# Kernel optimization log

Hardware: AMD Instinct MI355X
Metric: run time of the kernel (lower is better)

## Reference

```python
import jax, jax.numpy as jnp
import numpy as np

B, N, DS, DP, H, DH = 2, 512, 384, 128, 16, 64
MAX_SEQ = 2048
DI = H * DH  # inner attention dim = 1024
LN_EPS = 1e-5


def setup_inputs() -> dict:
    key = jax.random.key(0)
    ks = jax.random.split(key, 10)
    s = 0.02  # param init scale
    return {
        "single_repr": jax.random.normal(ks[0], (B, N, DS), jnp.float32),
        "pairwise_repr": jax.random.normal(ks[1], (B, N, N, DP), jnp.float32),
        "ln_gamma": jnp.ones((DP,), jnp.float32),
        "ln_beta": jnp.zeros((DP,), jnp.float32),
        "w_bias": jax.random.normal(ks[2], (DP, H), jnp.float32) * s,
        "attn_bias_bias": jax.random.normal(ks[3], (MAX_SEQ, MAX_SEQ), jnp.float32) * s,
        "w_q": jax.random.normal(ks[4], (DS, DI), jnp.float32) * s,
        "w_k": jax.random.normal(ks[5], (DS, DI), jnp.float32) * s,
        "w_v": jax.random.normal(ks[6], (DS, DI), jnp.float32) * s,
        "w_g": jax.random.normal(ks[7], (DS, DI), jnp.float32) * s,
        "w_o": jax.random.normal(ks[8], (DI, DS), jnp.float32) * s,
    }


def reference(single_repr, pairwise_repr, ln_gamma, ln_beta, w_bias,
              attn_bias_bias, w_q, w_k, w_v, w_g, w_o):
    b, n, _ = single_repr.shape
    # LayerNorm over pairwise feature dim, then project to per-head bias
    mu = pairwise_repr.mean(-1, keepdims=True)
    var = pairwise_repr.var(-1, keepdims=True)
    pr = (pairwise_repr - mu) * jax.lax.rsqrt(var + LN_EPS) * ln_gamma + ln_beta
    # ... i j h -> ... h i j, plus learned positional bias slice
    attn_bias = jnp.einsum('bijd,dh->bhij', pr, w_bias) + attn_bias_bias[:n, :n]

    # multi-head attention with additive per-head bias and sigmoid gating
    q = (single_repr @ w_q).reshape(b, n, H, DH).transpose(0, 2, 1, 3)  # bhnd
    k = (single_repr @ w_k).reshape(b, n, H, DH).transpose(0, 2, 1, 3)
    v = (single_repr @ w_v).reshape(b, n, H, DH).transpose(0, 2, 1, 3)
    scale = DH ** -0.5
    scores = jnp.einsum('bhid,bhjd->bhij', q, k) * scale + attn_bias
    attn = jax.nn.softmax(scores, axis=-1)
    o = jnp.einsum('bhij,bhjd->bhid', attn, v)
    o = o.transpose(0, 2, 1, 3).reshape(b, n, DI)
    gates = jax.nn.sigmoid(single_repr @ w_g)
    return (o * gates) @ w_o
```

## Files before the change

### kernel.cpp

```cpp
#include <hip/hip_runtime.h>
#include <hip/hip_bf16.h>

#define B_ 2
#define N_ 512
#define DS_ 384
#define DP_ 128
#define H_ 16
#define DH_ 64
#define DI_ 1024
#define MAXSEQ 2048
#define PAD 8

typedef float f32x4 __attribute__((ext_vector_type(4)));
typedef short bf16x8 __attribute__((ext_vector_type(8)));

__device__ __forceinline__ unsigned short f2b(float f) {
    unsigned int u = __builtin_bit_cast(unsigned int, f);
    u += 0x7FFFu + ((u >> 16) & 1u);
    return (unsigned short)(u >> 16);
}
__device__ __forceinline__ float b2f(unsigned short s) {
    unsigned int u = ((unsigned int)s) << 16;
    return __builtin_bit_cast(float, u);
}

__global__ __launch_bounds__(256) void k_transpose_all(const float* __restrict__ wq,
                                                       const float* __restrict__ wk,
                                                       const float* __restrict__ wv,
                                                       const float* __restrict__ wg,
                                                       const float* __restrict__ wo,
                                                       const float* __restrict__ gamma,
                                                       const float* __restrict__ beta,
                                                       const float* __restrict__ wb,
                                                       unsigned short* __restrict__ Wt,
                                                       unsigned short* __restrict__ Wot,
                                                       unsigned short* __restrict__ GhG,
                                                       float* __restrict__ SsG,
                                                       float* __restrict__ TsG) {
    int z = blockIdx.z;
    if (z == 5) {
        if (blockIdx.x || blockIdx.y) return;
        int t = threadIdx.x;
        for (int idx = t; idx < DP_ * H_; idx += 256) {
            int d = idx >> 4, h = idx & 15;
            GhG[h * DP_ + d] = f2b(gamma[d] * wb[idx]);
        }
        if (t < 32) {
            int h = t & 15;
            const float* src = (t >= 16) ? beta : gamma;
            float s = 0.f;
            for (int d = 0; d < DP_; ++d) s = fmaf(src[d], wb[d * H_ + h], s);
            if (t >= 16) TsG[h] = s; else SsG[h] = s;
        }
        return;
    }
    __shared__ float tile[32][33];
    const float* in;
    unsigned short* out;
    int R, C;
    if (z < 4) {
        in = (z == 0) ? wq : (z == 1) ? wk : (z == 2) ? wv : wg;
        out = Wt + (long)z * 1024 * 384;
        R = 384; C = 1024;
    } else {
        in = wo; out = Wot; R = 1024; C = 384;
    }
    int c0 = blockIdx.x * 32, r0 = blockIdx.y * 32;
    if (c0 >= C || r0 >= R) return;
    int tx = threadIdx.x & 31, ty = threadIdx.x >> 5;
    #pragma unroll
    for (int i = ty; i < 32; i += 8)
        tile[i][tx] = in[(long)(r0 + i) * C + (c0 + tx)];
    __syncthreads();
    #pragma unroll
    for (int i = ty; i < 32; i += 8)
        out[(long)(c0 + i) * R + (r0 + tx)] = f2b(tile[tx][i]);
}

__global__ __launch_bounds__(256) void k_bias(const float* __restrict__ pw,
                                              const float* __restrict__ abb,
                                              const unsigned short* __restrict__ GhG,
                                              const float* __restrict__ SsG,
                                              const float* __restrict__ TsG,
                                              unsigned short* __restrict__ biasP) {
    __shared__ float Xs[64 * 128];
    __shared__ float rsum[4][16] __attribute__((aligned(16)));
    __shared__ float rsq[4][16] __attribute__((aligned(16)));
    int t = threadIdx.x;
    int w = t >> 6, lane = t & 63;
    int lane15 = lane & 15, kg = lane >> 4;
    long p0 = (long)blockIdx.x * 64;
    int i_blk = (int)((p0 >> 9) & (N_ - 1));
    int j0 = (int)(p0 & (N_ - 1));
    long bb = p0 >> 18;

    const char* src = (const char*)(pw + (p0 << 7));
    char* lds = (char*)Xs;
    #pragma unroll
    for (int c = 0; c < 8; ++c) {
        int L = c * 4096 + t * 16;
        int row = L >> 9, b = L & 511;
        uint4 v = *(const uint4*)(src + L);
        *(uint4*)(lds + (row << 9) + (b ^ ((row & 7) << 4))) = v;
    }

    bf16x8 gb[4];
    #pragma unroll
    for (int kk = 0; kk < 4; ++kk)
        gb[kk] = *(const bf16x8*)&GhG[lane15 * DP_ + kk * 32 + kg * 8];
    float sh = SsG[lane15], th = TsG[lane15];
    __syncthreads();

    int row = w * 16 + lane15;
    const char* rbase = lds + (row << 9);
    int sw = (lane15 & 7) << 4;
    f32x4 xa[4], xb4[4];
    #pragma unroll
    for (int kk = 0; kk < 4; ++kk) {
        int b0 = kk * 128 + kg * 32;
        xa[kk]  = *(const f32x4*)(rbase + ((b0) ^ sw));
        xb4[kk] = *(const f32x4*)(rbase + ((b0 + 16) ^ sw));
    }
    float s = 0.f, q = 0.f;
    #pragma unroll
    for (int kk = 0; kk < 4; ++kk) {
        s += xa[kk][0] + xa[kk][1] + xa[kk][2] + xa[kk][3];
        s += xb4[kk][0] + xb4[kk][1] + xb4[kk][2] + xb4[kk][3];
        #pragma unroll
        for (int e = 0; e < 4; ++e) {
            q = fmaf(xa[kk][e], xa[kk][e], q);
            q = fmaf(xb4[kk][e], xb4[kk][e], q);
        }
    }
    s += __shfl_xor(s, 16); s += __shfl_xor(s, 32);
    q += __shfl_xor(q, 16); q += __shfl_xor(q, 32);
    if (lane < 16) { rsum[w][lane15] = s; rsq[w][lane15] = q; }

    f32x4 acc = {};
    #pragma unroll
    for (int kk = 0; kk < 4; ++kk) {
        bf16x8 a;
        unsigned short* ap = (unsigned short*)&a;
        ap[0] = f2b(xa[kk][0]);  ap[1] = f2b(xa[kk][1]);
        ap[2] = f2b(xa[kk][2]);  ap[3] = f2b(xa[kk][3]);
        ap[4] = f2b(xb4[kk][0]); ap[5] = f2b(xb4[kk][1]);
        ap[6] = f2b(xb4[kk][2]); ap[7] = f2b(xb4[kk][3]);
        acc = __builtin_amdgcn_mfma_f32_16x16x32_bf16(a, gb[kk], acc, 0, 0, 0);
    }
    int jr = w * 16 + kg * 4;
    float4 rs = *(const float4*)&rsum[w][kg * 4];
    float4 rq = *(const float4*)&rsq[w][kg * 4];
    float4 av = *(const float4*)(abb + (long)i_blk * MAXSEQ + j0 + jr);
    unsigned short* planeBase = biasP + ((bb * H_ + lane15) * N_ + i_blk) * N_ + j0;
    ushort4 res;
    float mu, var;
    mu = rs.x * (1.f / DP_); var = fmaf(rq.x, 1.f / DP_, -mu * mu);
    res.x = f2b(fmaf(rsqrtf(var + 1e-5f), acc[0] - mu * sh, th + av.x));
    mu = rs.y * (1.f / DP_); var = fmaf(rq.y, 1.f / DP_, -mu * mu);
    res.y = f2b(fmaf(rsqrtf(var + 1e-5f), acc[1] - mu * sh, th + av.y));
    mu = rs.z * (1.f / DP_); var = fmaf(rq.z, 1.f / DP_, -mu * mu);
    res.z = f2b(fmaf(rsqrtf(var + 1e-5f), acc[2] - mu * sh, th + av.z));
    mu = rs.w * (1.f / DP_); var = fmaf(rq.w, 1.f / DP_, -mu * mu);
    res.w = f2b(fmaf(rsqrtf(var + 1e-5f), acc[3] - mu * sh, th + av.w));
    *(ushort4*)(planeBase + jr) = res;
}

__global__ __launch_bounds__(256) void k_proj(const float* __restrict__ X,
                                              const unsigned short* __restrict__ Wt,
                                              unsigned short* __restrict__ Qb,
                                              unsigned short* __restrict__ Kb,
                                              unsigned short* __restrict__ Vt,
                                              unsigned short* __restrict__ Xg) {
    __shared__ unsigned short As[128][64 + PAD];
    __shared__ unsigned short Bs[128][64 + PAD];
    int m0 = blockIdx.x * 128;
    int n0 = blockIdx.y * 128;
    int t = threadIdx.x;
    int wave = t >> 6, lane = t & 63;
    int wr = wave >> 1, wc = wave & 1;
    int lane15 = lane & 15, kg = lane >> 4;
    f32x4 acc[4][4] = {};
    for (int k0 = 0; k0 < DS_; k0 += 64) {
        __syncthreads();
        {
            int r = t >> 1, half = t & 1;
            const float4* src = (const float4*)(X + (long)(m0 + r) * DS_ + k0 + half * 32);
            unsigned short* dst = &As[r][half * 32];
            #pragma unroll
            for (int ii = 0; ii < 8; ++ii) {
                float4 v = src[ii];
                dst[ii * 4 + 0] = f2b(v.x); dst[ii * 4 + 1] = f2b(v.y);
                dst[ii * 4 + 2] = f2b(v.z); dst[ii * 4 + 3] = f2b(v.w);
            }
            const uint4* wsrc = (const uint4*)(Wt + (long)(n0 + r) * DS_ + k0 + half * 32);
            uint4* wdst = (uint4*)&Bs[r][half * 32];
            wdst[0] = wsrc[0]; wdst[1] = wsrc[1]; wdst[2] = wsrc[2]; wdst[3] = wsrc[3];
        }
        __syncthreads();
        #pragma unroll
        for (int ks = 0; ks < 2; ++ks) {
            bf16x8 a[4], bb[4];
            #pragma unroll
            for (int mf = 0; mf < 4; ++mf)
                a[mf] = *(const bf16x8*)&As[wr * 64 + mf * 16 + lane15][ks * 32 + kg * 8];
            #pragma unroll
            for (int nf = 0; nf < 4; ++nf)
                bb[nf] = *(const bf16x8*)&Bs[wc * 64 + nf * 16 + lane15][ks * 32 + kg * 8];
            #pragma unroll
            for (int mf = 0; mf < 4; ++mf)
                #pragma unroll
                for (int nf = 0; nf < 4; ++nf)
                    acc[mf][nf] = __builtin_amdgcn_mfma_f32_16x16x32_bf16(a[mf], bb[nf], acc[mf][nf], 0, 0, 0);
        }
    }
    int p = n0 >> 10;
    int lgrp = lane >> 4;
    #pragma unroll
    for (int mf = 0; mf < 4; ++mf) {
        #pragma unroll
        for (int nf = 0; nf < 4; ++nf) {
            int col = n0 + wc * 64 + nf * 16 + lane15;
            int ch = col & 1023;
            int h = ch >> 6, dh = ch & 63;
            int row0 = m0 + wr * 64 + mf * 16 + lgrp * 4;
            if (p == 0 || p == 1) {
                unsigned short* base = (p == 0) ? Qb : Kb;
                float scl = (p == 0) ? 0.125f : 1.0f;
                #pragma unroll
                for (int r = 0; r < 4; ++r) {
                    int row = row0 + r;
                    int b = row >> 9, n = row & 511;
                    base[(((long)(b * 16 + h)) * 512 + n) * 64 + dh] = f2b(acc[mf][nf][r] * scl);
                }
            } else if (p == 2) {
                int b = row0 >> 9, n = row0 & 511;
                ushort4 v;
                v.x = f2b(acc[mf][nf][0]); v.y = f2b(acc[mf][nf][1]);
                v.z = f2b(acc[mf][nf][2]); v.w = f2b(acc[mf][nf][3]);
                *(ushort4*)&Vt[(((long)(b * 16 + h)) * 64 + dh) * 512 + n] = v;
            } else {
                #pragma unroll
                for (int r = 0; r < 4; ++r) {
                    int row = row0 + r;
                    Xg[(long)row * 1024 + ch] = f2b(acc[mf][nf][r]);
                }
            }
        }
    }
}

__global__ __launch_bounds__(256) void k_flash(const unsigned short* __restrict__ Qb,
                                               const unsigned short* __restrict__ Kb,
                                               const unsigned short* __restrict__ Vt,
                                               const unsigned short* __restrict__ biasP,
                                               const unsigned short* __restrict__ Xg,
                                               unsigned short* __restrict__ Og) {
    __shared__ unsigned short Kt[64][72];
    __shared__ unsigned short Vs[64][72];
    __shared__ unsigned short Bt[64][72];
    __shared__ unsigned short Ps[4][16][72];
    int bh = blockIdx.y;
    int b = bh >> 4, h = bh & 15;
    int i0 = blockIdx.x * 64;
    int t = threadIdx.x, w = t >> 6, lane = t & 63;
    int lane15 = lane & 15, lgrp = lane >> 4;

    bf16x8 qf[2];
    #pragma unroll
    for (int kk = 0; kk < 2; ++kk)
        qf[kk] = *(const bf16x8*)&Qb[((long)bh * 512 + i0 + w * 16 + lane15) * 64 + kk * 32 + lgrp * 8];

    float m_run = -1e30f, l_run = 0.f;
    f32x4 o[4] = {};

    for (int jt = 0; jt < 8; ++jt) {
        int j0 = jt * 64;
        __syncthreads();
        #pragma unroll
        for (int i = 0; i < 2; ++i) {
            int f = i * 256 + t;
            int r = f >> 3, c = f & 7;
            *(uint4*)&Kt[r][c * 8] = *(const uint4*)&Kb[((long)bh * 512 + j0 + r) * 64 + c * 8];
            *(uint4*)&Vs[r][c * 8] = *(const uint4*)&Vt[((long)bh * 64 + r) * 512 + j0 + c * 8];
            *(uint4*)&Bt[r][c * 8] = *(const uint4*)&biasP[(((long)bh * 512) + i0 + r) * 512 + j0 + c * 8];
        }
        __syncthreads();

        f32x4 s[4];
        #pragma unroll
        for (int nf = 0; nf < 4; ++nf) {
            f32x4 z = {};
            #pragma unroll
            for (int kk = 0; kk < 2; ++kk) {
                bf16x8 af = *(const bf16x8*)&Kt[nf * 16 + lane15][kk * 32 + lgrp * 8];
                z = __builtin_amdgcn_mfma_f32_16x16x32_bf16(af, qf[kk], z, 0, 0, 0);
            }
            s[nf] = z;
        }
        #pragma unroll
        for (int nf = 0; nf < 4; ++nf)
            #pragma unroll
            for (int r = 0; r < 4; ++r)
                s[nf][r] += b2f(Bt[w * 16 + lane15][nf * 16 + lgrp * 4 + r]);

        float pmax = s[0][0];
        #pragma unroll
        for (int nf = 0; nf < 4; ++nf)
            #pragma unroll
            for (int r = 0; r < 4; ++r) pmax = fmaxf(pmax, s[nf][r]);
        pmax = fmaxf(pmax, __shfl_xor(pmax, 16));
        pmax = fmaxf(pmax, __shfl_xor(pmax, 32));
        float m_new = fmaxf(m_run, pmax);
        float scale = __expf(m_run - m_new);
        float psum = 0.f;
        #pragma unroll
        for (int nf = 0; nf < 4; ++nf)
            #pragma unroll
            for (int r = 0; r < 4; ++r) {
                s[nf][r] = __expf(s[nf][r] - m_new);
                psum += s[nf][r];
            }
        psum += __shfl_xor(psum, 16);
        psum += __shfl_xor(psum, 32);
        l_run = l_run * scale + psum;
        m_run = m_new;
        #pragma unroll
        for (int r = 0; r < 4; ++r) {
            float sc = __shfl(scale, lgrp * 4 + r);
            #pragma unroll
            for (int nf = 0; nf < 4; ++nf) o[nf][r] *= sc;
        }
        #pragma unroll
        for (int nf = 0; nf < 4; ++nf)
            #pragma unroll
            for (int r = 0; r < 4; ++r)
                Ps[w][lane15][nf * 16 + lgrp * 4 + r] = f2b(s[nf][r]);
        #pragma unroll
        for (int kk = 0; kk < 2; ++kk) {
            bf16x8 pa = *(const bf16x8*)&Ps[w][lane15][kk * 32 + lgrp * 8];
            #pragma unroll
            for (int nf = 0; nf < 4; ++nf) {
                bf16x8 vb = *(const bf16x8*)&Vs[nf * 16 + lane15][kk * 32 + lgrp * 8];
                o[nf] = __builtin_amdgcn_mfma_f32_16x16x32_bf16(pa, vb, o[nf], 0, 0, 0);
            }
        }
    }
    #pragma unroll
    for (int r = 0; r < 4; ++r) {
        float l_r = __shfl(l_run, lgrp * 4 + r);
        float inv = 1.f / l_r;
        long grow = (long)b * 512 + i0 + w * 16 + lgrp * 4 + r;
        #pragma unroll
        for (int nf = 0; nf < 4; ++nf) {
            int dh = nf * 16 + lane15;
            float xgv = b2f(Xg[grow * 1024 + h * 64 + dh]);
            float gate = 1.f / (1.f + __expf(-xgv));
            Og[grow * 1024 + h * 64 + dh] = f2b(o[nf][r] * inv * gate);
        }
    }
}

__global__ __launch_bounds__(256) void k_out(const unsigned short* __restrict__ Og,
                                             const unsigned short* __restrict__ Wot,
                                             float* __restrict__ out) {
    __shared__ unsigned short As[128][64 + PAD];
    __shared__ unsigned short Bs[128][64 + PAD];
    int m0 = blockIdx.x * 128, n0 = blockIdx.y * 128;
    int t = threadIdx.x, wave = t >> 6, lane = t & 63;
    int wr = wave >> 1, wc = wave & 1;
    int lane15 = lane & 15, kg = lane >> 4;
    f32x4 acc[4][4] = {};
    for (int k0 = 0; k0 < 1024; k0 += 64) {
        __syncthreads();
        {
            int r = t >> 1, half = t & 1;
            const uint4* src = (const uint4*)(Og + (long)(m0 + r) * 1024 + k0 + half * 32);
            uint4* dst = (uint4*)&As[r][half * 32];
            dst[0] = src[0]; dst[1] = src[1]; dst[2] = src[2]; dst[3] = src[3];
            const uint4* wsrc = (const uint4*)(Wot + (long)(n0 + r) * 1024 + k0 + half * 32);
            uint4* wdst = (uint4*)&Bs[r][half * 32];
            wdst[0] = wsrc[0]; wdst[1] = wsrc[1]; wdst[2] = wsrc[2]; wdst[3] = wsrc[3];
        }
        __syncthreads();
        #pragma unroll
        for (int ks = 0; ks < 2; ++ks) {
            bf16x8 a[4], bb[4];
            #pragma unroll
            for (int mf = 0; mf < 4; ++mf)
                a[mf] = *(const bf16x8*)&As[wr * 64 + mf * 16 + lane15][ks * 32 + kg * 8];
            #pragma unroll
            for (int nf = 0; nf < 4; ++nf)
                bb[nf] = *(const bf16x8*)&Bs[wc * 64 + nf * 16 + lane15][ks * 32 + kg * 8];
            #pragma unroll
            for (int mf = 0; mf < 4; ++mf)
                #pragma unroll
                for (int nf = 0; nf < 4; ++nf)
                    acc[mf][nf] = __builtin_amdgcn_mfma_f32_16x16x32_bf16(a[mf], bb[nf], acc[mf][nf], 0, 0, 0);
        }
    }
    int lgrp = lane >> 4;
    #pragma unroll
    for (int mf = 0; mf < 4; ++mf) {
        #pragma unroll
        for (int nf = 0; nf < 4; ++nf) {
            int col = n0 + wc * 64 + nf * 16 + lane15;
            int row0 = m0 + wr * 64 + mf * 16 + lgrp * 4;
            #pragma unroll
            for (int r = 0; r < 4; ++r)
                out[(long)(row0 + r) * DS_ + col] = acc[mf][nf][r];
        }
    }
}

extern "C" void kernel_launch(void* const* d_in, const int* in_sizes, int n_in,
                              void* d_out, int out_size, void* d_ws, size_t ws_size,
                              hipStream_t stream) {
    const float* single = (const float*)d_in[0];
    const float* pw     = (const float*)d_in[1];
    const float* gamma  = (const float*)d_in[2];
    const float* beta   = (const float*)d_in[3];
    const float* wb     = (const float*)d_in[4];
    const float* abb    = (const float*)d_in[5];
    const float* wq     = (const float*)d_in[6];
    const float* wk     = (const float*)d_in[7];
    const float* wv     = (const float*)d_in[8];
    const float* wg     = (const float*)d_in[9];
    const float* wo     = (const float*)d_in[10];
    float* out = (float*)d_out;
    char* ws = (char*)d_ws;

    unsigned short* SP  = (unsigned short*)(ws);
    unsigned short* Qb  = (unsigned short*)(ws + 16777216);
    unsigned short* Kb  = (unsigned short*)(ws + 18874368);
    unsigned short* Vt  = (unsigned short*)(ws + 20971520);
    unsigned short* Xg  = (unsigned short*)(ws + 23068672);
    unsigned short* Og  = (unsigned short*)(ws + 25165824);
    unsigned short* Wt  = (unsigned short*)(ws + 27262976);
    unsigned short* Wot = (unsigned short*)(ws + 30408704);
    unsigned short* GhG = (unsigned short*)(ws + 31195136);
    float* SsG          = (float*)(ws + 31199232);
    float* TsG          = (float*)(ws + 31199296);

    k_transpose_all<<<dim3(32, 32, 6), 256, 0, stream>>>(wq, wk, wv, wg, wo,
                                                         gamma, beta, wb,
                                                         Wt, Wot, GhG, SsG, TsG);
    k_bias<<<8192, 256, 0, stream>>>(pw, abb, GhG, SsG, TsG, SP);
    k_proj<<<dim3(8, 32), 256, 0, stream>>>(single, Wt, Qb, Kb, Vt, Xg);
    k_flash<<<dim3(8, 32), 256, 0, stream>>>(Qb, Kb, Vt, SP, Xg, Og);
    k_out<<<dim3(8, 3), 256, 0, stream>>>(Og, Wot, out);
}
```

Before: 132.8 us.

## Prefetch next tiles into registers and use direct global-to-LDS loads

```diff
diff --git a/kernel.cpp b/kernel.cpp
--- a/kernel.cpp
+++ b/kernel.cpp
@@ -13,6 +13,8 @@
 
 typedef float f32x4 __attribute__((ext_vector_type(4)));
 typedef short bf16x8 __attribute__((ext_vector_type(8)));
+typedef const __attribute__((address_space(1))) unsigned int ga_u32;
+typedef __attribute__((address_space(3))) unsigned int ld_u32;
 
 __device__ __forceinline__ unsigned short f2b(float f) {
     unsigned int u = __builtin_bit_cast(unsigned int, f);
@@ -94,14 +96,17 @@
     int j0 = (int)(p0 & (N_ - 1));
     long bb = p0 >> 18;
 
-    const char* src = (const char*)(pw + (p0 << 7));
-    char* lds = (char*)Xs;
-    #pragma unroll
-    for (int c = 0; c < 8; ++c) {
-        int L = c * 4096 + t * 16;
-        int row = L >> 9, b = L & 511;
-        uint4 v = *(const uint4*)(src + L);
-        *(uint4*)(lds + (row << 9) + (b ^ ((row & 7) << 4))) = v;
+    {
+        const char* src = (const char*)(pw + (p0 << 7));
+        #pragma unroll
+        for (int c = 0; c < 8; ++c) {
+            int L = (w * 8 + c) * 1024 + lane * 16;
+            int row = L >> 9, bp = L & 511;
+            const char* gaddr = src + ((row << 9) | (bp ^ ((row & 7) << 4)));
+            __builtin_amdgcn_global_load_lds((ga_u32*)gaddr,
+                                             (ld_u32*)((char*)Xs + (w * 8 + c) * 1024),
+                                             16, 0, 0);
+        }
     }
 
     bf16x8 gb[4];
@@ -112,7 +117,7 @@
     __syncthreads();
 
     int row = w * 16 + lane15;
-    const char* rbase = lds + (row << 9);
+    const char* rbase = (const char*)Xs + (row << 9);
     int sw = (lane15 & 7) << 4;
     f32x4 xa[4], xb4[4];
     #pragma unroll
@@ -179,24 +184,39 @@
     int wave = t >> 6, lane = t & 63;
     int wr = wave >> 1, wc = wave & 1;
     int lane15 = lane & 15, kg = lane >> 4;
+    int r = t >> 1, half = t & 1;
     f32x4 acc[4][4] = {};
+    float4 xr[8];
+    uint4 wreg[4];
+    {
+        const float4* src = (const float4*)(X + (long)(m0 + r) * DS_ + half * 32);
+        #pragma unroll
+        for (int ii = 0; ii < 8; ++ii) xr[ii] = src[ii];
+        const uint4* wsrc = (const uint4*)(Wt + (long)(n0 + r) * DS_ + half * 32);
+        #pragma unroll
+        for (int ii = 0; ii < 4; ++ii) wreg[ii] = wsrc[ii];
+    }
     for (int k0 = 0; k0 < DS_; k0 += 64) {
         __syncthreads();
         {
-            int r = t >> 1, half = t & 1;
-            const float4* src = (const float4*)(X + (long)(m0 + r) * DS_ + k0 + half * 32);
             unsigned short* dst = &As[r][half * 32];
             #pragma unroll
             for (int ii = 0; ii < 8; ++ii) {
-                float4 v = src[ii];
-                dst[ii * 4 + 0] = f2b(v.x); dst[ii * 4 + 1] = f2b(v.y);
-                dst[ii * 4 + 2] = f2b(v.z); dst[ii * 4 + 3] = f2b(v.w);
+                dst[ii * 4 + 0] = f2b(xr[ii].x); dst[ii * 4 + 1] = f2b(xr[ii].y);
+                dst[ii * 4 + 2] = f2b(xr[ii].z); dst[ii * 4 + 3] = f2b(xr[ii].w);
             }
-            const uint4* wsrc = (const uint4*)(Wt + (long)(n0 + r) * DS_ + k0 + half * 32);
             uint4* wdst = (uint4*)&Bs[r][half * 32];
-            wdst[0] = wsrc[0]; wdst[1] = wsrc[1]; wdst[2] = wsrc[2]; wdst[3] = wsrc[3];
-        }
-        __syncthreads();
+            wdst[0] = wreg[0]; wdst[1] = wreg[1]; wdst[2] = wreg[2]; wdst[3] = wreg[3];
+        }
+        __syncthreads();
+        if (k0 + 64 < DS_) {
+            const float4* src = (const float4*)(X + (long)(m0 + r) * DS_ + k0 + 64 + half * 32);
+            #pragma unroll
+            for (int ii = 0; ii < 8; ++ii) xr[ii] = src[ii];
+            const uint4* wsrc = (const uint4*)(Wt + (long)(n0 + r) * DS_ + k0 + 64 + half * 32);
+            #pragma unroll
+            for (int ii = 0; ii < 4; ++ii) wreg[ii] = wsrc[ii];
+        }
         #pragma unroll
         for (int ks = 0; ks < 2; ++ks) {
             bf16x8 a[4], bb[4];
@@ -227,10 +247,10 @@
                 unsigned short* base = (p == 0) ? Qb : Kb;
                 float scl = (p == 0) ? 0.125f : 1.0f;
                 #pragma unroll
-                for (int r = 0; r < 4; ++r) {
-                    int row = row0 + r;
-                    int b = row >> 9, n = row & 511;
-                    base[(((long)(b * 16 + h)) * 512 + n) * 64 + dh] = f2b(acc[mf][nf][r] * scl);
+                for (int rr = 0; rr < 4; ++rr) {
+                    int rowx = row0 + rr;
+                    int b = rowx >> 9, n = rowx & 511;
+                    base[(((long)(b * 16 + h)) * 512 + n) * 64 + dh] = f2b(acc[mf][nf][rr] * scl);
                 }
             } else if (p == 2) {
                 int b = row0 >> 9, n = row0 & 511;
@@ -240,9 +260,9 @@
                 *(ushort4*)&Vt[(((long)(b * 16 + h)) * 64 + dh) * 512 + n] = v;
             } else {
                 #pragma unroll
-                for (int r = 0; r < 4; ++r) {
-                    int row = row0 + r;
-                    Xg[(long)row * 1024 + ch] = f2b(acc[mf][nf][r]);
+                for (int rr = 0; rr < 4; ++rr) {
+                    int rowx = row0 + rr;
+                    Xg[(long)rowx * 1024 + ch] = f2b(acc[mf][nf][rr]);
                 }
             }
         }
@@ -264,6 +284,8 @@
     int i0 = blockIdx.x * 64;
     int t = threadIdx.x, w = t >> 6, lane = t & 63;
     int lane15 = lane & 15, lgrp = lane >> 4;
+    int r0_ = t >> 3, c0_ = t & 7;
+    int r1_ = (256 + t) >> 3, c1_ = t & 7;
 
     bf16x8 qf[2];
     #pragma unroll
@@ -273,18 +295,26 @@
     float m_run = -1e30f, l_run = 0.f;
     f32x4 o[4] = {};
 
+    uint4 rk[2], rv[2], rb[2];
+#define FL_LOAD(JT) do { int jq = (JT) * 64; \
+    rk[0] = *(const uint4*)&Kb[((long)bh * 512 + jq + r0_) * 64 + c0_ * 8]; \
+    rv[0] = *(const uint4*)&Vt[((long)bh * 64 + r0_) * 512 + jq + c0_ * 8]; \
+    rb[0] = *(const uint4*)&biasP[(((long)bh * 512) + i0 + r0_) * 512 + jq + c0_ * 8]; \
+    rk[1] = *(const uint4*)&Kb[((long)bh * 512 + jq + r1_) * 64 + c1_ * 8]; \
+    rv[1] = *(const uint4*)&Vt[((long)bh * 64 + r1_) * 512 + jq + c1_ * 8]; \
+    rb[1] = *(const uint4*)&biasP[(((long)bh * 512) + i0 + r1_) * 512 + jq + c1_ * 8]; } while (0)
+
+    FL_LOAD(0);
     for (int jt = 0; jt < 8; ++jt) {
-        int j0 = jt * 64;
-        __syncthreads();
-        #pragma unroll
-        for (int i = 0; i < 2; ++i) {
-            int f = i * 256 + t;
-            int r = f >> 3, c = f & 7;
-            *(uint4*)&Kt[r][c * 8] = *(const uint4*)&Kb[((long)bh * 512 + j0 + r) * 64 + c * 8];
-            *(uint4*)&Vs[r][c * 8] = *(const uint4*)&Vt[((long)bh * 64 + r) * 512 + j0 + c * 8];
-            *(uint4*)&Bt[r][c * 8] = *(const uint4*)&biasP[(((long)bh * 512) + i0 + r) * 512 + j0 + c * 8];
-        }
-        __syncthreads();
+        __syncthreads();
+        *(uint4*)&Kt[r0_][c0_ * 8] = rk[0];
+        *(uint4*)&Vs[r0_][c0_ * 8] = rv[0];
+        *(uint4*)&Bt[r0_][c0_ * 8] = rb[0];
+        *(uint4*)&Kt[r1_][c1_ * 8] = rk[1];
+        *(uint4*)&Vs[r1_][c1_ * 8] = rv[1];
+        *(uint4*)&Bt[r1_][c1_ * 8] = rb[1];
+        __syncthreads();
+        if (jt < 7) FL_LOAD(jt + 1);
 
         f32x4 s[4];
         #pragma unroll
@@ -298,16 +328,17 @@
             s[nf] = z;
         }
         #pragma unroll
+        for (int nf = 0; nf < 4; ++nf) {
+            ushort4 bv = *(const ushort4*)&Bt[w * 16 + lane15][nf * 16 + lgrp * 4];
+            s[nf][0] += b2f(bv.x); s[nf][1] += b2f(bv.y);
+            s[nf][2] += b2f(bv.z); s[nf][3] += b2f(bv.w);
+        }
+
+        float pmax = s[0][0];
+        #pragma unroll
         for (int nf = 0; nf < 4; ++nf)
             #pragma unroll
-            for (int r = 0; r < 4; ++r)
-                s[nf][r] += b2f(Bt[w * 16 + lane15][nf * 16 + lgrp * 4 + r]);
-
-        float pmax = s[0][0];
-        #pragma unroll
-        for (int nf = 0; nf < 4; ++nf)
-            #pragma unroll
-            for (int r = 0; r < 4; ++r) pmax = fmaxf(pmax, s[nf][r]);
+            for (int rr = 0; rr < 4; ++rr) pmax = fmaxf(pmax, s[nf][rr]);
         pmax = fmaxf(pmax, __shfl_xor(pmax, 16));
         pmax = fmaxf(pmax, __shfl_xor(pmax, 32));
         float m_new = fmaxf(m_run, pmax);
@@ -316,25 +347,27 @@
         #pragma unroll
         for (int nf = 0; nf < 4; ++nf)
             #pragma unroll
-            for (int r = 0; r < 4; ++r) {
-                s[nf][r] = __expf(s[nf][r] - m_new);
-                psum += s[nf][r];
+            for (int rr = 0; rr < 4; ++rr) {
+                s[nf][rr] = __expf(s[nf][rr] - m_new);
+                psum += s[nf][rr];
             }
         psum += __shfl_xor(psum, 16);
         psum += __shfl_xor(psum, 32);
         l_run = l_run * scale + psum;
         m_run = m_new;
         #pragma unroll
-        for (int r = 0; r < 4; ++r) {
-            float sc = __shfl(scale, lgrp * 4 + r);
-            #pragma unroll
-            for (int nf = 0; nf < 4; ++nf) o[nf][r] *= sc;
-        }
-        #pragma unroll
-        for (int nf = 0; nf < 4; ++nf)
-            #pragma unroll
-            for (int r = 0; r < 4; ++r)
-                Ps[w][lane15][nf * 16 + lgrp * 4 + r] = f2b(s[nf][r]);
+        for (int rr = 0; rr < 4; ++rr) {
+            float sc = __shfl(scale, lgrp * 4 + rr);
+            #pragma unroll
+            for (int nf = 0; nf < 4; ++nf) o[nf][rr] *= sc;
+        }
+        #pragma unroll
+        for (int nf = 0; nf < 4; ++nf) {
+            ushort4 pv_;
+            pv_.x = f2b(s[nf][0]); pv_.y = f2b(s[nf][1]);
+            pv_.z = f2b(s[nf][2]); pv_.w = f2b(s[nf][3]);
+            *(ushort4*)&Ps[w][lane15][nf * 16 + lgrp * 4] = pv_;
+        }
         #pragma unroll
         for (int kk = 0; kk < 2; ++kk) {
             bf16x8 pa = *(const bf16x8*)&Ps[w][lane15][kk * 32 + lgrp * 8];
@@ -345,17 +378,18 @@
             }
         }
     }
-    #pragma unroll
-    for (int r = 0; r < 4; ++r) {
-        float l_r = __shfl(l_run, lgrp * 4 + r);
+#undef FL_LOAD
+    #pragma unroll
+    for (int rr = 0; rr < 4; ++rr) {
+        float l_r = __shfl(l_run, lgrp * 4 + rr);
         float inv = 1.f / l_r;
-        long grow = (long)b * 512 + i0 + w * 16 + lgrp * 4 + r;
+        long grow = (long)b * 512 + i0 + w * 16 + lgrp * 4 + rr;
         #pragma unroll
         for (int nf = 0; nf < 4; ++nf) {
             int dh = nf * 16 + lane15;
             float xgv = b2f(Xg[grow * 1024 + h * 64 + dh]);
             float gate = 1.f / (1.f + __expf(-xgv));
-            Og[grow * 1024 + h * 64 + dh] = f2b(o[nf][r] * inv * gate);
+            Og[grow * 1024 + h * 64 + dh] = f2b(o[nf][rr] * inv * gate);
         }
     }
 }
@@ -369,19 +403,30 @@
     int t = threadIdx.x, wave = t >> 6, lane = t & 63;
     int wr = wave >> 1, wc = wave & 1;
     int lane15 = lane & 15, kg = lane >> 4;
+    int r = t >> 1, half = t & 1;
     f32x4 acc[4][4] = {};
+    uint4 ar[4], br[4];
+    {
+        const uint4* src = (const uint4*)(Og + (long)(m0 + r) * 1024 + half * 32);
+        const uint4* wsrc = (const uint4*)(Wot + (long)(n0 + r) * 1024 + half * 32);
+        #pragma unroll
+        for (int ii = 0; ii < 4; ++ii) { ar[ii] = src[ii]; br[ii] = wsrc[ii]; }
+    }
     for (int k0 = 0; k0 < 1024; k0 += 64) {
         __syncthreads();
         {
-            int r = t >> 1, half = t & 1;
-            const uint4* src = (const uint4*)(Og + (long)(m0 + r) * 1024 + k0 + half * 32);
             uint4* dst = (uint4*)&As[r][half * 32];
-            dst[0] = src[0]; dst[1] = src[1]; dst[2] = src[2]; dst[3] = src[3];
-            const uint4* wsrc = (const uint4*)(Wot + (long)(n0 + r) * 1024 + k0 + half * 32);
             uint4* wdst = (uint4*)&Bs[r][half * 32];
-            wdst[0] = wsrc[0]; wdst[1] = wsrc[1]; wdst[2] = wsrc[2]; wdst[3] = wsrc[3];
-        }
-        __syncthreads();
+            #pragma unroll
+            for (int ii = 0; ii < 4; ++ii) { dst[ii] = ar[ii]; wdst[ii] = br[ii]; }
+        }
+        __syncthreads();
+        if (k0 + 64 < 1024) {
+            const uint4* src = (const uint4*)(Og + (long)(m0 + r) * 1024 + k0 + 64 + half * 32);
+            const uint4* wsrc = (const uint4*)(Wot + (long)(n0 + r) * 1024 + k0 + 64 + half * 32);
+            #pragma unroll
+            for (int ii = 0; ii < 4; ++ii) { ar[ii] = src[ii]; br[ii] = wsrc[ii]; }
+        }
         #pragma unroll
         for (int ks = 0; ks < 2; ++ks) {
             bf16x8 a[4], bb[4];
@@ -406,8 +451,8 @@
             int col = n0 + wc * 64 + nf * 16 + lane15;
             int row0 = m0 + wr * 64 + mf * 16 + lgrp * 4;
             #pragma unroll
-            for (int r = 0; r < 4; ++r)
-                out[(long)(row0 + r) * DS_ + col] = acc[mf][nf][r];
+            for (int rr = 0; rr < 4; ++rr)
+                out[(long)(row0 + rr) * DS_ + col] = acc[mf][nf][rr];
         }
     }
 }
```

New measurement: 166.7 us. 1.26x slower.
